# Kernel optimization log

Measured on AMD Instinct MI355X. Metric: run time of the kernel, lower is better.

The kernel has to match this reference:

```python
import jax, jax.numpy as jnp
import numpy as np

_SQRT1_2 = 0.7071067811865476

B, S, D, N, NCH = 4, 2048, 1024, 32768, 8


def setup_inputs() -> dict:
    key = jax.random.key(0)
    ks = jax.random.split(key, 6)
    return {
        "x": jax.random.normal(ks[0], (B, S, D), jnp.float32),
        "h": jax.random.normal(ks[1], (B, S, D), jnp.float32),
        "emb": jax.random.normal(ks[2], (N, D), jnp.float32),
        "tau_offset": jax.random.normal(ks[3], (B, S, 1), jnp.float32),
        "w_read": jax.random.normal(ks[4], (N, D), jnp.float32),
        "w_write": jax.random.normal(ks[5], (N, D), jnp.float32),
        "n_chunks": NCH,
    }


def _srw_chunked(x, h, emb_unit, tau_offset, w_read, w_write, n_chunks):
    b, s, d = x.shape
    n = emb_unit.shape[0]
    cs = n // n_chunks
    h_bf = h.astype(jnp.bfloat16)
    x_bf = x.astype(jnp.bfloat16)
    emb_bf = emb_unit.astype(jnp.bfloat16)
    read_bf = w_read.astype(jnp.bfloat16)
    write_bf = w_write.astype(jnp.bfloat16)
    z1 = jnp.zeros((b, s, 1), jnp.float32)

    # ---- pass 1: online score statistics over chunks of N ----
    @jax.checkpoint
    def stats_step(carry, i):
        s_sum, sq_sum, cube_sum, ns_sum, ns_sq = carry
        ec = jax.lax.dynamic_slice_in_dim(emb_bf, i * cs, cs, axis=0)
        sc = (h_bf @ ec.T).astype(jnp.float32)  # [B,S,cs]
        s_sum = s_sum + sc.sum(-1, keepdims=True)
        sq_sum = sq_sum + (sc ** 2).sum(-1, keepdims=True)
        cube_sum = cube_sum + (sc ** 3).sum(-1, keepdims=True)
        pns = sc.mean(axis=(0, 1))  # per-neuron mean score [cs]
        return ((s_sum, sq_sum, cube_sum, ns_sum + pns.sum(), ns_sq + (pns ** 2).sum()), None)

    (s_sum, sq_sum, cube_sum, ns_sum, ns_sq), _ = jax.lax.scan(
        stats_step, (z1, z1, z1, jnp.float32(0.0), jnp.float32(0.0)), jnp.arange(n_chunks))

    s_mean = s_sum / n
    s_std = jnp.sqrt(sq_sum / n - s_mean ** 2) + 1e-08
    tau = s_mean + tau_offset * s_std
    cube_mean = cube_sum / n
    central_third = cube_mean - 3.0 * s_mean * s_std ** 2 - s_mean ** 3
    score_skew = jax.lax.stop_gradient((central_third / (s_std ** 3 + 1e-08)).mean())
    mean_score = ns_sum / n
    var_score = ns_sq / n - mean_score ** 2
    score_lb = var_score / (mean_score ** 2 + var_score + 0.01)

    # ---- pass 2: erf-threshold gate + read/write GEMM accumulate ----
    @jax.checkpoint
    def gate_step(carry, i):
        out, wcost, gmax, act, strong, phib, zsum, z075c, z030c, glg = carry
        s0 = i * cs
        ec = jax.lax.dynamic_slice_in_dim(emb_bf, s0, cs, axis=0)
        rc = jax.lax.dynamic_slice_in_dim(read_bf, s0, cs, axis=0)
        wc = jax.lax.dynamic_slice_in_dim(write_bf, s0, cs, axis=0)
        rc = rc / (jnp.linalg.norm(rc, axis=-1, keepdims=True) + 1e-08)
        wc = wc / (jnp.linalg.norm(wc, axis=-1, keepdims=True) + 1e-08)
        z = ((h_bf @ ec.T).astype(jnp.float32) - tau) / s_std  # [B,S,cs]
        phi = 0.5 * (1.0 + jax.lax.erf(z * _SQRT1_2))
        gate = jnp.where(z > 0, z * phi, 0.0)
        xr = x_bf @ rc.T  # [B,S,cs]
        c_out = ((gate.astype(jnp.bfloat16) * xr) @ wc).astype(jnp.float32)  # [B,S,D]
        g_safe = gate + 1e-08
        new = (
            out + c_out,
            wcost + gate.sum(-1, keepdims=True),
            jnp.maximum(gmax, gate.max(-1, keepdims=True)),
            act + (gate > 0.0).astype(jnp.float32).sum(-1, keepdims=True),
            strong + (gate > 0.5).astype(jnp.float32).sum(-1, keepdims=True),
            phib + ((phi > 0.95) | (phi < 0.05)).astype(jnp.float32).sum(-1, keepdims=True),
            zsum + jnp.where(z > 0, z, 0.0).sum(-1, keepdims=True),
            z075c + ((z > 0) & (z < 0.75)).astype(jnp.float32).sum(-1, keepdims=True),
            z030c + ((z > 0) & (z < 0.3)).astype(jnp.float32).sum(-1, keepdims=True),
            glg + (gate * jnp.log(g_safe)).sum(-1, keepdims=True),
        )
        return (new, None)

    init = (jnp.zeros((b, s, d), jnp.float32), z1, jnp.full((b, s, 1), -1e9, jnp.float32),
            z1, z1, z1, z1, z1, z1, z1)
    (raw_out, wcost, gmax, act, strong, phib, zsum, z075c, z030c, glg), _ = jax.lax.scan(
        gate_step, init, jnp.arange(n_chunks))

    den = jnp.maximum(wcost, 1.0)
    out = (raw_out / den).astype(jnp.bfloat16)
    score_std_out = s_std.mean()
    es_out = wcost.mean()
    active_n_mean = act.mean()
    z_mean_active = zsum / (act + 1e-08)
    active_eps = act + 1e-08
    z_lt_075_frac = jax.lax.stop_gradient((z075c / active_eps).mean())
    z_lt_030_frac = jax.lax.stop_gradient((z030c / active_eps).mean())
    tau_abs_mean = jax.lax.stop_gradient(tau).mean()
    active_per_token_std = jax.lax.stop_gradient(act).std()
    gate_sum_eps = wcost + 1e-08
    entropy_per_token = -glg / gate_sum_eps + jnp.log(gate_sum_eps)
    gate_entropy = jax.lax.stop_gradient(entropy_per_token).mean()
    return (out.astype(jnp.float32), act / n, gmax, score_lb, score_std_out, es_out,
            active_n_mean, strong / n, phib / n, z_mean_active, tau_abs_mean,
            z_lt_075_frac, z_lt_030_frac, score_skew, active_per_token_std, gate_entropy)


def reference(x, h, emb, tau_offset, w_read, w_write, n_chunks):
    emb_unit = emb / (jnp.linalg.norm(emb, axis=-1, keepdims=True) + 1e-08)
    return _srw_chunked(x, h, emb_unit, tau_offset, w_read, w_write, n_chunks)
```

## Files before the change

### kernel.cpp

```cpp
#include <hip/hip_runtime.h>

#define DEV __device__ __forceinline__

typedef __attribute__((ext_vector_type(4))) float f32x4;
typedef __attribute__((ext_vector_type(8))) short s16x8;

static const int NTOK = 8192;
static const int DD   = 1024;
static const int NNEU = 32768;

static const int OUT_ACT    = 8388608;
static const int OUT_GMAX   = 8396800;
static const int OUT_SLB    = 8404992;
static const int OUT_SSTD   = 8404993;
static const int OUT_ES     = 8404994;
static const int OUT_ANM    = 8404995;
static const int OUT_STRONG = 8404996;
static const int OUT_PHIB   = 8413188;
static const int OUT_ZMEAN  = 8421380;
static const int OUT_TAUM   = 8429572;
static const int OUT_Z75    = 8429573;
static const int OUT_Z30    = 8429574;
static const int OUT_SKEW   = 8429575;
static const int OUT_ASTD   = 8429576;
static const int OUT_ENT    = 8429577;

DEV unsigned short f2bf(float f){
  unsigned u = __float_as_uint(f);
  u += 0x7fffu + ((u >> 16) & 1u);
  return (unsigned short)(u >> 16);
}
DEV float bf2f(unsigned short h){ return __uint_as_float(((unsigned)h) << 16); }
DEV float rnd_bf(float f){ return bf2f(f2bf(f)); }

template<int AUX>
DEV void gl_lds16(const void* g, void* l){
  __builtin_amdgcn_global_load_lds(
      (const __attribute__((address_space(1))) unsigned int*)g,
      (__attribute__((address_space(3))) unsigned int*)l, 16, 0, AUX);
}

DEV f32x4 mfma16(s16x8 a, s16x8 b, f32x4 c){
  return __builtin_amdgcn_mfma_f32_16x16x32_bf16(a, b, c, 0, 0, 0);
}

template<int AUX>
DEV void stage4(const unsigned short* __restrict__ G, size_t ld, int k0,
                unsigned short* L, int t){
  #pragma unroll
  for (int i = 0; i < 4; i++){
    int ch = i*256 + t;
    int row = ch >> 3, c = ch & 7;
    int cs = c ^ (row & 7);
    int wb = (i*256 + (t & 192)) * 16;
    gl_lds16<AUX>(G + (size_t)row * ld + k0 + cs*8, (char*)L + wb);
  }
}

DEV s16x8 frg(const unsigned short* L, int R, int kk, int lq){
  int cc = ((kk >> 3) + lq) ^ (R & 7);
  return *(const s16x8*)((const char*)L + R*128 + cc*16);
}

DEV int2 xcd_remap(){
  int orig = blockIdx.y * gridDim.x + blockIdx.x;
  int nwg  = gridDim.x * gridDim.y;
  int q = nwg >> 3;
  int xcd = orig & 7, idx = orig >> 3;
  int pos = xcd * q + idx;
  int2 r; r.x = pos >> 6; r.y = pos & 63;
  return r;
}


__global__ __launch_bounds__(256) void k_norms(const float* __restrict__ e,
    const float* __restrict__ r_, const float* __restrict__ w_,
    float* __restrict__ inv_e, float* __restrict__ inv_r, float* __restrict__ inv_w){
  int t = threadIdx.x, l = t & 63, wv = t >> 6;
  int row = blockIdx.x * 4 + wv;
  const float4* ep = (const float4*)(e  + (size_t)row * DD);
  const float4* rp = (const float4*)(r_ + (size_t)row * DD);
  const float4* wp = (const float4*)(w_ + (size_t)row * DD);
  float se = 0.f, sr = 0.f, sw = 0.f;
  #pragma unroll
  for (int j = 0; j < 4; j++){
    float4 v = ep[j*64 + l];
    se += v.x*v.x + v.y*v.y + v.z*v.z + v.w*v.w;
    float4 a = rp[j*64 + l];
    float a0 = rnd_bf(a.x), a1 = rnd_bf(a.y), a2 = rnd_bf(a.z), a3 = rnd_bf(a.w);
    sr += a0*a0 + a1*a1 + a2*a2 + a3*a3;
    float4 c = wp[j*64 + l];
    float c0 = rnd_bf(c.x), c1 = rnd_bf(c.y), c2 = rnd_bf(c.z), c3 = rnd_bf(c.w);
    sw += c0*c0 + c1*c1 + c2*c2 + c3*c3;
  }
  #pragma unroll
  for (int d = 1; d < 64; d <<= 1){
    se += __shfl_xor(se, d); sr += __shfl_xor(sr, d); sw += __shfl_xor(sw, d);
  }
  if (l == 0){
    inv_e[row] = 1.f / (sqrtf(se) + 1e-8f);
    inv_r[row] = 1.f / (sqrtf(sr) + 1e-8f);
    inv_w[row] = 1.f / (sqrtf(sw) + 1e-8f);
  }
}

__global__ __launch_bounds__(256) void k_cast_scale(const float* __restrict__ in,
    const float* __restrict__ inv, unsigned short* __restrict__ o, int round_first){
  size_t i = (size_t)blockIdx.x * 256 + threadIdx.x;
  int row = (int)(i >> 8);
  float s = inv[row];
  float4 v = ((const float4*)in)[i];
  ushort4 r;
  if (round_first){
    r.x = f2bf(rnd_bf(v.x) * s); r.y = f2bf(rnd_bf(v.y) * s);
    r.z = f2bf(rnd_bf(v.z) * s); r.w = f2bf(rnd_bf(v.w) * s);
  } else {
    r.x = f2bf(v.x * s); r.y = f2bf(v.y * s);
    r.z = f2bf(v.z * s); r.w = f2bf(v.w * s);
  }
  ((ushort4*)o)[i] = r;
}

__global__ __launch_bounds__(256) void k_cast(const float* __restrict__ in,
                                              unsigned short* __restrict__ o){
  size_t i = (size_t)blockIdx.x * 256 + threadIdx.x;
  float4 v = ((const float4*)in)[i];
  ushort4 r;
  r.x = f2bf(v.x); r.y = f2bf(v.y); r.z = f2bf(v.z); r.w = f2bf(v.w);
  ((ushort4*)o)[i] = r;
}

__global__ __launch_bounds__(256) void k_wcnT(const float* __restrict__ w_,
    const float* __restrict__ invw, unsigned short* __restrict__ o){
  __shared__ unsigned short tile[64][65];
  int t = threadIdx.x;
  int n0b = blockIdx.x * 64, d0 = blockIdx.y * 64;
  #pragma unroll
  for (int i = 0; i < 16; i++){
    int idx = t + i*256;
    int r = idx >> 6, c = idx & 63;
    float v = w_[(size_t)(n0b + r) * DD + d0 + c];
    tile[c][r] = f2bf(rnd_bf(v) * invw[n0b + r]);
  }
  __syncthreads();
  #pragma unroll
  for (int i = 0; i < 16; i++){
    int idx = t + i*256;
    int rd = idx >> 6, cn = idx & 63;
    o[(size_t)(d0 + rd) * NNEU + n0b + cn] = tile[rd][cn];
  }
}

__global__ __launch_bounds__(256) void k_hsum(const unsigned short* __restrict__ hb,
                                              float* __restrict__ hs){
  int t = threadIdx.x; int r0 = blockIdx.x * 128;
  float s[4] = {0.f, 0.f, 0.f, 0.f};
  for (int r = 0; r < 128; r++){
    const unsigned short* row = hb + (size_t)(r0 + r) * DD;
    #pragma unroll
    for (int j = 0; j < 4; j++) s[j] += bf2f(row[j*256 + t]);
  }
  #pragma unroll
  for (int j = 0; j < 4; j++) atomicAdd(hs + j*256 + t, s[j]);
}

__global__ __launch_bounds__(256) void k_pns(const unsigned short* __restrict__ eb,
    const float* __restrict__ hs, float* __restrict__ ns){
  __shared__ float hsh[1024];
  __shared__ float pr[8];
  int t = threadIdx.x, l = t & 63, wv = t >> 6;
  for (int i = t; i < 1024; i += 256) hsh[i] = hs[i];
  __syncthreads();
  float bs = 0.f, bq = 0.f;
  for (int it = 0; it < 32; it++){
    int row = blockIdx.x * 128 + it*4 + wv;
    const unsigned short* er = eb + (size_t)row * DD + l*16;
    float s = 0.f;
    #pragma unroll
    for (int j = 0; j < 16; j++) s += hsh[l*16 + j] * bf2f(er[j]);
    #pragma unroll
    for (int d = 1; d < 64; d <<= 1) s += __shfl_xor(s, d);
    float pns = s * (1.f / 8192.f);
    bs += pns; bq += pns * pns;
  }
  if (l == 0){ pr[wv*2] = bs; pr[wv*2 + 1] = bq; }
  __syncthreads();
  if (t == 0){
    atomicAdd(ns + 0, pr[0] + pr[2] + pr[4] + pr[6]);
    atomicAdd(ns + 1, pr[1] + pr[3] + pr[5] + pr[7]);
  }
}


__global__ __launch_bounds__(256, 2) void k_stats_gemm(
    const unsigned short* __restrict__ A, const unsigned short* __restrict__ Bm,
    float* __restrict__ s_sum, float* __restrict__ sq_sum, float* __restrict__ cu_sum)
{
  __shared__ unsigned short lds[16384];
  unsigned short* lA = lds;
  unsigned short* lB = lds + 8192;
  const int t = threadIdx.x, l = t & 63, wv = t >> 6;
  const int wm = wv >> 1, wn = wv & 1;
  const int lq = l >> 4, lr = l & 15;
  int2 rm = xcd_remap();
  const int bx = rm.x, by = rm.y;
  const unsigned short* Ab = A  + (size_t)by * 128 * DD;
  const unsigned short* Bb = Bm + (size_t)bx * 128 * DD;
  f32x4 acc[4][4];
  #pragma unroll
  for (int m = 0; m < 4; m++)
    #pragma unroll
    for (int n = 0; n < 4; n++) acc[m][n] = (f32x4){0.f, 0.f, 0.f, 0.f};

  for (int k0 = 0; k0 < DD; k0 += 64){
    __syncthreads();
    stage4<0>(Ab, DD, k0, lA, t);
    stage4<0>(Bb, DD, k0, lB, t);
    asm volatile("s_waitcnt vmcnt(0)" ::: "memory");
    __syncthreads();
    #pragma unroll
    for (int kk = 0; kk < 64; kk += 32){
      s16x8 af[4], bf4[4];
      #pragma unroll
      for (int m = 0; m < 4; m++) af[m]  = frg(lA, wm*64 + m*16 + lr, kk, lq);
      #pragma unroll
      for (int n = 0; n < 4; n++) bf4[n] = frg(lB, wn*64 + n*16 + lr, kk, lq);
      #pragma unroll
      for (int m = 0; m < 4; m++)
        #pragma unroll
        for (int n = 0; n < 4; n++)
          acc[m][n] = mfma16(af[m], bf4[n], acc[m][n]);
    }
  }
  __syncthreads();
  float* red = (float*)lds;
  #pragma unroll
  for (int m = 0; m < 4; m++)
  #pragma unroll
  for (int r = 0; r < 4; r++){
    float s1 = 0.f, s2 = 0.f, s3 = 0.f;
    #pragma unroll
    for (int n = 0; n < 4; n++){
      float v = rnd_bf(acc[m][n][r]);
      s1 += v; float v2 = v*v; s2 += v2; s3 += v2*v;
    }
    #pragma unroll
    for (int d = 1; d < 16; d <<= 1){
      s1 += __shfl_xor(s1, d); s2 += __shfl_xor(s2, d); s3 += __shfl_xor(s3, d);
    }
    if (lr == 0){
      int rl = wm*64 + m*16 + lq*4 + r;
      float* p = red + (wn*128 + rl)*4;
      p[0] = s1; p[1] = s2; p[2] = s3;
    }
  }
  __syncthreads();
  const int row0 = by * 128;
  for (int idx = t; idx < 384; idx += 256){
    int rl = idx / 3, st = idx - rl*3;
    float v = red[rl*4 + st] + red[(128 + rl)*4 + st];
    float* dst = (st == 0) ? s_sum : (st == 1) ? sq_sum : cu_sum;
    atomicAdd(dst + row0 + rl, v);
  }
}

__global__ __launch_bounds__(256) void k_tau(const float* __restrict__ s_sum,
    const float* __restrict__ sq_sum, const float* __restrict__ tof,
    float* __restrict__ tau, float* __restrict__ rstd){
  int i = blockIdx.x * 256 + threadIdx.x;
  float mean = s_sum[i] * (1.f / 32768.f);
  float var  = sq_sum[i] * (1.f / 32768.f) - mean*mean;
  float sstd = sqrtf(fmaxf(var, 0.f)) + 1e-8f;
  tau[i]  = mean + tof[i] * sstd;
  rstd[i] = 1.f / sstd;
}


__global__ __launch_bounds__(256, 2) void k_gate_gemm(
    const unsigned short* __restrict__ Hb, const unsigned short* __restrict__ Eb,
    const unsigned short* __restrict__ Xb, const unsigned short* __restrict__ Rb,
    const float* __restrict__ tau, const float* __restrict__ rstd,
    unsigned short* __restrict__ P, int NC, int n0,
    float* __restrict__ wcostp, float* __restrict__ gmaxp, float* __restrict__ actp,
    float* __restrict__ strongp, float* __restrict__ phibp, float* __restrict__ zsump,
    float* __restrict__ z075p, float* __restrict__ z030p, float* __restrict__ glgp)
{
  __shared__ unsigned short lds[32768];
  unsigned short* lH = lds;
  unsigned short* lE = lds + 8192;
  unsigned short* lX = lds + 16384;
  unsigned short* lR = lds + 24576;
  const int t = threadIdx.x, l = t & 63, wv = t >> 6;
  const int wm = wv >> 1, wn = wv & 1;
  const int lq = l >> 4, lr = l & 15;
  int2 rm = xcd_remap();
  const int bx = rm.x, by = rm.y;
  const unsigned short* Hp = Hb + (size_t)by * 128 * DD;
  const unsigned short* Xp = Xb + (size_t)by * 128 * DD;
  const unsigned short* Ep = Eb + (size_t)(n0 + bx*128) * DD;
  const unsigned short* Rp = Rb + (size_t)(n0 + bx*128) * DD;
  f32x4 accS[4][4], accX[4][4];
  #pragma unroll
  for (int m = 0; m < 4; m++)
    #pragma unroll
    for (int n = 0; n < 4; n++){
      accS[m][n] = (f32x4){0.f,0.f,0.f,0.f};
      accX[m][n] = (f32x4){0.f,0.f,0.f,0.f};
    }

  for (int k0 = 0; k0 < DD; k0 += 64){
    __syncthreads();
    stage4<0>(Hp, DD, k0, lH, t);
    stage4<0>(Ep, DD, k0, lE, t);
    stage4<0>(Xp, DD, k0, lX, t);
    stage4<0>(Rp, DD, k0, lR, t);
    asm volatile("s_waitcnt vmcnt(0)" ::: "memory");
    __syncthreads();
    #pragma unroll
    for (int kk = 0; kk < 64; kk += 32){
      s16x8 af[4], bf4[4];
      #pragma unroll
      for (int m = 0; m < 4; m++) af[m]  = frg(lH, wm*64 + m*16 + lr, kk, lq);
      #pragma unroll
      for (int n = 0; n < 4; n++) bf4[n] = frg(lE, wn*64 + n*16 + lr, kk, lq);
      #pragma unroll
      for (int m = 0; m < 4; m++)
        #pragma unroll
        for (int n = 0; n < 4; n++)
          accS[m][n] = mfma16(af[m], bf4[n], accS[m][n]);
      #pragma unroll
      for (int m = 0; m < 4; m++) af[m]  = frg(lX, wm*64 + m*16 + lr, kk, lq);
      #pragma unroll
      for (int n = 0; n < 4; n++) bf4[n] = frg(lR, wn*64 + n*16 + lr, kk, lq);
      #pragma unroll
      for (int m = 0; m < 4; m++)
        #pragma unroll
        for (int n = 0; n < 4; n++)
          accX[m][n] = mfma16(af[m], bf4[n], accX[m][n]);
    }
  }
  __syncthreads();
  float* red = (float*)lds;
  #pragma unroll
  for (int m = 0; m < 4; m++)
  #pragma unroll
  for (int r = 0; r < 4; r++){
    int rl = wm*64 + m*16 + lq*4 + r;
    int gr = by*128 + rl;
    float tauv = tau[gr], rs = rstd[gr];
    float wsum = 0.f, gmx = 0.f, ac = 0.f, stc = 0.f, pb = 0.f;
    float zs = 0.f, z7 = 0.f, z3 = 0.f, gl = 0.f;
    #pragma unroll
    for (int n = 0; n < 4; n++){
      float sc = rnd_bf(accS[m][n][r]);
      float xr = rnd_bf(accX[m][n][r]);
      float z = (sc - tauv) * rs;
      float phi = 0.5f * (1.0f + erff(z * 0.70710678118654752440f));
      float gate = (z > 0.f) ? z * phi : 0.f;
      wsum += gate; gmx = fmaxf(gmx, gate);
      if (gate > 0.f)  ac  += 1.f;
      if (gate > 0.5f) stc += 1.f;
      if (phi > 0.95f || phi < 0.05f) pb += 1.f;
      if (z > 0.f){ zs += z; if (z < 0.75f) z7 += 1.f; if (z < 0.3f) z3 += 1.f; }
      gl += gate * __logf(gate + 1e-8f);
      float p = rnd_bf(gate) * xr;
      __builtin_nontemporal_store(f2bf(p), &P[(size_t)gr * NC + bx*128 + wn*64 + n*16 + lr]);
    }
    #pragma unroll
    for (int d = 1; d < 16; d <<= 1){
      wsum += __shfl_xor(wsum, d); gmx = fmaxf(gmx, __shfl_xor(gmx, d));
      ac += __shfl_xor(ac, d);  stc += __shfl_xor(stc, d); pb += __shfl_xor(pb, d);
      zs += __shfl_xor(zs, d);  z7  += __shfl_xor(z7, d);  z3 += __shfl_xor(z3, d);
      gl += __shfl_xor(gl, d);
    }
    if (lr == 0){
      float* p = red + (wn*128 + rl)*10;
      p[0]=wsum; p[1]=gmx; p[2]=ac; p[3]=stc; p[4]=pb; p[5]=zs; p[6]=z7; p[7]=z3; p[8]=gl;
    }
  }
  __syncthreads();
  for (int idx = t; idx < 1152; idx += 256){
    int rl = idx / 9, st = idx - rl*9;
    float a = red[rl*10 + st], b = red[(128 + rl)*10 + st];
    int gr = by*128 + rl;
    if (st == 1){
      atomicMax((int*)(gmaxp + gr), __float_as_int(fmaxf(a, b)));
    } else {
      float v = a + b;
      float* dst = (st==0)?wcostp:(st==2)?actp:(st==3)?strongp:(st==4)?phibp:
                   (st==5)?zsump:(st==6)?z075p:(st==7)?z030p:glgp;
      atomicAdd(dst + gr, v);
    }
  }
}


__global__ __launch_bounds__(256, 2) void k_out_gemm(
    const unsigned short* __restrict__ Pm, const unsigned short* __restrict__ Bt,
    float* __restrict__ outp, int NC, int n0, int accum)
{
  __shared__ unsigned short lds[16384];
  unsigned short* lA = lds;
  unsigned short* lB = lds + 8192;
  const int t = threadIdx.x, l = t & 63, wv = t >> 6;
  const int wm = wv >> 1, wn = wv & 1;
  const int lq = l >> 4, lr = l & 15;
  int2 rm = xcd_remap();
  const int bx = rm.x, by = rm.y;
  const unsigned short* Ab = Pm + (size_t)by * 128 * NC;
  const unsigned short* Bb = Bt + (size_t)bx * 128 * NNEU + n0;
  f32x4 acc[4][4];
  #pragma unroll
  for (int m = 0; m < 4; m++)
    #pragma unroll
    for (int n = 0; n < 4; n++) acc[m][n] = (f32x4){0.f,0.f,0.f,0.f};

  for (int k0 = 0; k0 < NC; k0 += 64){
    __syncthreads();
    stage4<2>(Ab, NC, k0, lA, t);
    stage4<0>(Bb, NNEU, k0, lB, t);
    asm volatile("s_waitcnt vmcnt(0)" ::: "memory");
    __syncthreads();
    #pragma unroll
    for (int kk = 0; kk < 64; kk += 32){
      s16x8 af[4], bf4[4];
      #pragma unroll
      for (int m = 0; m < 4; m++) af[m]  = frg(lA, wm*64 + m*16 + lr, kk, lq);
      #pragma unroll
      for (int n = 0; n < 4; n++) bf4[n] = frg(lB, wn*64 + n*16 + lr, kk, lq);
      #pragma unroll
      for (int m = 0; m < 4; m++)
        #pragma unroll
        for (int n = 0; n < 4; n++)
          acc[m][n] = mfma16(af[m], bf4[n], acc[m][n]);
    }
  }
  #pragma unroll
  for (int m = 0; m < 4; m++)
  #pragma unroll
  for (int n = 0; n < 4; n++)
  #pragma unroll
  for (int r = 0; r < 4; r++){
    int gr = by*128 + wm*64 + m*16 + lq*4 + r;
    int dc = bx*128 + wn*64 + n*16 + lr;
    float* o = outp + (size_t)gr * DD + dc;
    if (accum) *o += acc[m][n][r];
    else       *o  = acc[m][n][r];
  }
}


__global__ __launch_bounds__(256) void k_out_fin(float* __restrict__ o,
                                                 const float* __restrict__ wcost){
  size_t i = (size_t)blockIdx.x * 256 + threadIdx.x;
  float4 v = ((const float4*)o)[i];
  int tk = (int)(i >> 8);
  float den = fmaxf(wcost[tk], 1.f);
  v.x = rnd_bf(v.x / den); v.y = rnd_bf(v.y / den);
  v.z = rnd_bf(v.z / den); v.w = rnd_bf(v.w / den);
  ((float4*)o)[i] = v;
}

__global__ __launch_bounds__(1024) void k_final(
    const float* __restrict__ s_sum, const float* __restrict__ sq_sum,
    const float* __restrict__ cu_sum, const float* __restrict__ tof,
    const float* __restrict__ wcost, const float* __restrict__ gmax,
    const float* __restrict__ act, const float* __restrict__ strong,
    const float* __restrict__ phib, const float* __restrict__ zsum,
    const float* __restrict__ z075, const float* __restrict__ z030,
    const float* __restrict__ glg, const float* __restrict__ ns,
    float* __restrict__ out)
{
  int tid = threadIdx.x;
  float s0=0,s1=0,s2=0,s3=0,s4=0,s5=0,s6=0,s7=0,s8=0;
  for (int i = tid; i < NTOK; i += 1024){
    float mean = s_sum[i] * (1.f / 32768.f);
    float var  = sq_sum[i] * (1.f / 32768.f) - mean*mean;
    float sstd = sqrtf(fmaxf(var, 0.f)) + 1e-8f;
    float tauv = mean + tof[i] * sstd;
    float wc = wcost[i], ac = act[i];
    out[OUT_ACT + i]    = ac * (1.f / 32768.f);
    out[OUT_GMAX + i]   = gmax[i];
    out[OUT_STRONG + i] = strong[i] * (1.f / 32768.f);
    out[OUT_PHIB + i]   = phib[i] * (1.f / 32768.f);
    out[OUT_ZMEAN + i]  = zsum[i] / (ac + 1e-8f);
    float c3 = cu_sum[i] * (1.f / 32768.f) - 3.f*mean*sstd*sstd - mean*mean*mean;
    float skew = c3 / (sstd*sstd*sstd + 1e-8f);
    float gse = wc + 1e-8f;
    float ent = -glg[i] / gse + logf(gse);
    s0 += sstd; s1 += wc; s2 += ac; s3 += ac*ac; s4 += tauv;
    s5 += z075[i] / (ac + 1e-8f); s6 += z030[i] / (ac + 1e-8f); s7 += skew; s8 += ent;
  }
  __shared__ float rb[16][9];
  int lane = tid & 63, wid = tid >> 6;
  #pragma unroll
  for (int d = 1; d < 64; d <<= 1){
    s0 += __shfl_xor(s0,d); s1 += __shfl_xor(s1,d); s2 += __shfl_xor(s2,d);
    s3 += __shfl_xor(s3,d); s4 += __shfl_xor(s4,d); s5 += __shfl_xor(s5,d);
    s6 += __shfl_xor(s6,d); s7 += __shfl_xor(s7,d); s8 += __shfl_xor(s8,d);
  }
  if (lane == 0){
    rb[wid][0]=s0; rb[wid][1]=s1; rb[wid][2]=s2; rb[wid][3]=s3; rb[wid][4]=s4;
    rb[wid][5]=s5; rb[wid][6]=s6; rb[wid][7]=s7; rb[wid][8]=s8;
  }
  __syncthreads();
  if (tid == 0){
    float S[9];
    for (int k = 0; k < 9; k++){ float a = 0.f; for (int w2 = 0; w2 < 16; w2++) a += rb[w2][k]; S[k] = a; }
    const float inv = 1.f / 8192.f;
    float act_mean = S[2] * inv;
    out[OUT_SSTD] = S[0] * inv;
    out[OUT_ES]   = S[1] * inv;
    out[OUT_ANM]  = act_mean;
    out[OUT_ASTD] = sqrtf(fmaxf(S[3]*inv - act_mean*act_mean, 0.f));
    out[OUT_TAUM] = S[4] * inv;
    out[OUT_Z75]  = S[5] * inv;
    out[OUT_Z30]  = S[6] * inv;
    out[OUT_SKEW] = S[7] * inv;
    out[OUT_ENT]  = S[8] * inv;
    float ms = ns[0] * (1.f / 32768.f);
    float vs = ns[1] * (1.f / 32768.f) - ms*ms;
    out[OUT_SLB] = vs / (ms*ms + vs + 0.01f);
  }
}


extern "C" void kernel_launch(void* const* d_in, const int* in_sizes, int n_in,
                              void* d_out, int out_size, void* d_ws, size_t ws_size,
                              hipStream_t stream)
{
  (void)in_sizes; (void)n_in; (void)out_size;
  const float* x   = (const float*)d_in[0];
  const float* h   = (const float*)d_in[1];
  const float* emb = (const float*)d_in[2];
  const float* tof = (const float*)d_in[3];
  const float* wr  = (const float*)d_in[4];
  const float* ww  = (const float*)d_in[5];
  float* out = (float*)d_out;
  char* ws = (char*)d_ws;

  size_t off = 0;
  auto get = [&](size_t n){ size_t o = off; off += (n + 255) & ~(size_t)255; return o; };
  unsigned short* emb_bf = (unsigned short*)(ws + get((size_t)NNEU*DD*2));
  unsigned short* rcn_bf = (unsigned short*)(ws + get((size_t)NNEU*DD*2));
  unsigned short* wcnT   = (unsigned short*)(ws + get((size_t)DD*NNEU*2));
  unsigned short* h_bf   = (unsigned short*)(ws + get((size_t)NTOK*DD*2));
  unsigned short* x_bf   = (unsigned short*)(ws + get((size_t)NTOK*DD*2));
  float* inv_e = (float*)(ws + get(NNEU*4));
  float* inv_r = (float*)(ws + get(NNEU*4));
  float* inv_w = (float*)(ws + get(NNEU*4));
  size_t zoff = off;
  float* hsum   = (float*)(ws + get(DD*4));
  float* s_sum  = (float*)(ws + get(NTOK*4));
  float* sq_sum = (float*)(ws + get(NTOK*4));
  float* cu_sum = (float*)(ws + get(NTOK*4));
  float* tau    = (float*)(ws + get(NTOK*4));
  float* rstd   = (float*)(ws + get(NTOK*4));
  float* wcost  = (float*)(ws + get(NTOK*4));
  float* gmax   = (float*)(ws + get(NTOK*4));
  float* act    = (float*)(ws + get(NTOK*4));
  float* strong = (float*)(ws + get(NTOK*4));
  float* phib   = (float*)(ws + get(NTOK*4));
  float* zsum   = (float*)(ws + get(NTOK*4));
  float* z075   = (float*)(ws + get(NTOK*4));
  float* z030   = (float*)(ws + get(NTOK*4));
  float* glg    = (float*)(ws + get(NTOK*4));
  float* ns     = (float*)(ws + get(256));
  size_t zlen = off - zoff;
  off = (off + 4095) & ~(size_t)4095;
  size_t poff = off;
  size_t pavail = ws_size > poff ? ws_size - poff : 0;
  int nsplit = 1;
  while (nsplit < 64 && (size_t)NTOK * (NNEU / nsplit) * 2 > pavail) nsplit <<= 1;
  int NC = NNEU / nsplit;
  unsigned short* P = (unsigned short*)(ws + poff);

  hipMemsetAsync(ws + zoff, 0, zlen, stream);

  dim3 b256(256);
  k_norms<<<dim3(NNEU/4), b256, 0, stream>>>(emb, wr, ww, inv_e, inv_r, inv_w);
  k_cast_scale<<<dim3(NNEU*DD/4/256), b256, 0, stream>>>(emb, inv_e, emb_bf, 0);
  k_cast_scale<<<dim3(NNEU*DD/4/256), b256, 0, stream>>>(wr, inv_r, rcn_bf, 1);
  k_wcnT<<<dim3(NNEU/64, DD/64), b256, 0, stream>>>(ww, inv_w, wcnT);
  k_cast<<<dim3(NTOK*DD/4/256), b256, 0, stream>>>(h, h_bf);
  k_cast<<<dim3(NTOK*DD/4/256), b256, 0, stream>>>(x, x_bf);
  k_hsum<<<dim3(NTOK/128), b256, 0, stream>>>(h_bf, hsum);
  k_pns<<<dim3(NNEU/128), b256, 0, stream>>>(emb_bf, hsum, ns);
  k_stats_gemm<<<dim3(NNEU/128, NTOK/128), b256, 0, stream>>>(h_bf, emb_bf, s_sum, sq_sum, cu_sum);
  k_tau<<<dim3(NTOK/256), b256, 0, stream>>>(s_sum, sq_sum, tof, tau, rstd);
  for (int c = 0; c < nsplit; ++c){
    k_gate_gemm<<<dim3(NC/128, NTOK/128), b256, 0, stream>>>(h_bf, emb_bf, x_bf, rcn_bf,
        tau, rstd, P, NC, c*NC, wcost, gmax, act, strong, phib, zsum, z075, z030, glg);
    k_out_gemm<<<dim3(DD/128, NTOK/128), b256, 0, stream>>>(P, wcnT, out, NC, c*NC, c);
  }
  k_out_fin<<<dim3(NTOK*DD/4/256), b256, 0, stream>>>(out, wcost);
  k_final<<<dim3(1), dim3(1024), 0, stream>>>(s_sum, sq_sum, cu_sum, tof, wcost, gmax,
      act, strong, phib, zsum, z075, z030, glg, ns, out);
}
```

Before: 4.118 ms.

## Cache bf16 score matrix from stats pass, double-buffer GEMM LDS loads

The stats GEMM now writes its bf16 score tile to workspace, so the gate pass reads cached scores instead of recomputing H·Eᵀ. It only computes the X·Rᵀ GEMM, with a fallback to the full gate GEMM when workspace is short. The stats, gate and output GEMMs get double-buffered LDS staging that prefetches the next k-tile during MFMA compute. The transposed write-weight buffer aliases emb_bf once it is dead, and the chunk size is fixed to four chunks. This trades an extra 512MB of score writes and reads for removing half the gate-pass FLOPs, and relies on the workspace being large enough.

```diff
diff --git a/kernel.cpp b/kernel.cpp
--- a/kernel.cpp
+++ b/kernel.cpp
@@ -4,10 +4,12 @@
 
 typedef __attribute__((ext_vector_type(4))) float f32x4;
 typedef __attribute__((ext_vector_type(8))) short s16x8;
+typedef __attribute__((ext_vector_type(8))) unsigned short u16x8;
 
 static const int NTOK = 8192;
 static const int DD   = 1024;
 static const int NNEU = 32768;
+static const int NC   = 8192;
 
 static const int OUT_ACT    = 8388608;
 static const int OUT_GMAX   = 8396800;
@@ -62,6 +64,12 @@
   return *(const s16x8*)((const char*)L + R*128 + cc*16);
 }
 
+DEV void waitv_bar(){
+  asm volatile("s_waitcnt vmcnt(0)" ::: "memory");
+  __builtin_amdgcn_s_barrier();
+  __builtin_amdgcn_sched_barrier(0);
+}
+
 DEV int2 xcd_remap(){
   int orig = blockIdx.y * gridDim.x + blockIdx.x;
   int nwg  = gridDim.x * gridDim.y;
@@ -194,11 +202,10 @@
 
 __global__ __launch_bounds__(256, 2) void k_stats_gemm(
     const unsigned short* __restrict__ A, const unsigned short* __restrict__ Bm,
-    float* __restrict__ s_sum, float* __restrict__ sq_sum, float* __restrict__ cu_sum)
+    float* __restrict__ s_sum, float* __restrict__ sq_sum, float* __restrict__ cu_sum,
+    unsigned short* __restrict__ Sb, int kst)
 {
-  __shared__ unsigned short lds[16384];
-  unsigned short* lA = lds;
-  unsigned short* lB = lds + 8192;
+  __shared__ unsigned short lds[32768];
   const int t = threadIdx.x, l = t & 63, wv = t >> 6;
   const int wm = wv >> 1, wn = wv & 1;
   const int lq = l >> 4, lr = l & 15;
@@ -212,27 +219,62 @@
     #pragma unroll
     for (int n = 0; n < 4; n++) acc[m][n] = (f32x4){0.f, 0.f, 0.f, 0.f};
 
-  for (int k0 = 0; k0 < DD; k0 += 64){
-    __syncthreads();
-    stage4<0>(Ab, DD, k0, lA, t);
-    stage4<0>(Bb, DD, k0, lB, t);
-    asm volatile("s_waitcnt vmcnt(0)" ::: "memory");
-    __syncthreads();
+  stage4<0>(Ab, DD, 0, lds, t);
+  stage4<0>(Bb, DD, 0, lds + 8192, t);
+  waitv_bar();
+  int cur = 0;
+  for (int ks = 0; ks < 16; ++ks){
+    unsigned short* Lc = lds + cur*16384;
+    if (ks + 1 < 16){
+      unsigned short* Ln = lds + (cur^1)*16384;
+      int k0 = (ks+1)*64;
+      stage4<0>(Ab, DD, k0, Ln, t);
+      stage4<0>(Bb, DD, k0, Ln + 8192, t);
+    }
     #pragma unroll
     for (int kk = 0; kk < 64; kk += 32){
       s16x8 af[4], bf4[4];
       #pragma unroll
-      for (int m = 0; m < 4; m++) af[m]  = frg(lA, wm*64 + m*16 + lr, kk, lq);
-      #pragma unroll
-      for (int n = 0; n < 4; n++) bf4[n] = frg(lB, wn*64 + n*16 + lr, kk, lq);
+      for (int m = 0; m < 4; m++) af[m]  = frg(Lc, wm*64 + m*16 + lr, kk, lq);
+      #pragma unroll
+      for (int n = 0; n < 4; n++) bf4[n] = frg(Lc + 8192, wn*64 + n*16 + lr, kk, lq);
       #pragma unroll
       for (int m = 0; m < 4; m++)
         #pragma unroll
         for (int n = 0; n < 4; n++)
           acc[m][n] = mfma16(af[m], bf4[n], acc[m][n]);
     }
-  }
-  __syncthreads();
+    waitv_bar();
+    cur ^= 1;
+  }
+
+  int ci = bx >> 6;
+  if (ci < kst){
+    unsigned short* sl = lds;
+    #pragma unroll
+    for (int m = 0; m < 4; m++)
+    #pragma unroll
+    for (int n = 0; n < 4; n++)
+    #pragma unroll
+    for (int r = 0; r < 4; r++){
+      int rl = wm*64 + m*16 + lq*4 + r;
+      int cl = wn*64 + n*16 + lr;
+      sl[rl*136 + cl] = f2bf(acc[m][n][r]);
+    }
+    __syncthreads();
+    unsigned short* Sp = Sb + (size_t)ci * NTOK * NC;
+    int bxc = bx & 63;
+    #pragma unroll
+    for (int i = 0; i < 8; i++){
+      int idx = i*2048 + t*8;
+      int row = idx >> 7, col = idx & 127;
+      u16x8 v = *(const u16x8*)&sl[row*136 + col];
+      __builtin_nontemporal_store(v,
+        (u16x8*)(Sp + (size_t)(by*128 + row) * NC + bxc*128 + col));
+    }
+  }
+  __syncthreads();
+
   float* red = (float*)lds;
   #pragma unroll
   for (int m = 0; m < 4; m++)
@@ -276,11 +318,130 @@
 }
 
 
+__global__ __launch_bounds__(256, 2) void k_gateS(
+    const unsigned short* __restrict__ Xb, const unsigned short* __restrict__ Rb,
+    const float* __restrict__ tau, const float* __restrict__ rstd,
+    unsigned short* __restrict__ SP, int n0,
+    float* __restrict__ wcostp, float* __restrict__ gmaxp, float* __restrict__ actp,
+    float* __restrict__ strongp, float* __restrict__ phibp, float* __restrict__ zsump,
+    float* __restrict__ z075p, float* __restrict__ z030p, float* __restrict__ glgp)
+{
+  __shared__ unsigned short lds[32768];
+  const int t = threadIdx.x, l = t & 63, wv = t >> 6;
+  const int wm = wv >> 1, wn = wv & 1;
+  const int lq = l >> 4, lr = l & 15;
+  int2 rm = xcd_remap();
+  const int bx = rm.x, by = rm.y;
+  const unsigned short* Xp = Xb + (size_t)by * 128 * DD;
+  const unsigned short* Rp = Rb + (size_t)(n0 + bx*128) * DD;
+  f32x4 accX[4][4];
+  #pragma unroll
+  for (int m = 0; m < 4; m++)
+    #pragma unroll
+    for (int n = 0; n < 4; n++) accX[m][n] = (f32x4){0.f,0.f,0.f,0.f};
+
+  stage4<0>(Xp, DD, 0, lds, t);
+  stage4<0>(Rp, DD, 0, lds + 8192, t);
+  waitv_bar();
+  int cur = 0;
+  for (int ks = 0; ks < 16; ++ks){
+    unsigned short* Lc = lds + cur*16384;
+    if (ks + 1 < 16){
+      unsigned short* Ln = lds + (cur^1)*16384;
+      int k0 = (ks+1)*64;
+      stage4<0>(Xp, DD, k0, Ln, t);
+      stage4<0>(Rp, DD, k0, Ln + 8192, t);
+    }
+    #pragma unroll
+    for (int kk = 0; kk < 64; kk += 32){
+      s16x8 af[4], bf4[4];
+      #pragma unroll
+      for (int m = 0; m < 4; m++) af[m]  = frg(Lc, wm*64 + m*16 + lr, kk, lq);
+      #pragma unroll
+      for (int n = 0; n < 4; n++) bf4[n] = frg(Lc + 8192, wn*64 + n*16 + lr, kk, lq);
+      #pragma unroll
+      for (int m = 0; m < 4; m++)
+        #pragma unroll
+        for (int n = 0; n < 4; n++)
+          accX[m][n] = mfma16(af[m], bf4[n], accX[m][n]);
+    }
+    waitv_bar();
+    cur ^= 1;
+  }
+
+  unsigned short sv[4][4][4];
+  #pragma unroll
+  for (int m = 0; m < 4; m++)
+  #pragma unroll
+  for (int r = 0; r < 4; r++)
+  #pragma unroll
+  for (int n = 0; n < 4; n++){
+    int gr = by*128 + wm*64 + m*16 + lq*4 + r;
+    int gc = bx*128 + wn*64 + n*16 + lr;
+    sv[m][r][n] = SP[(size_t)gr * NC + gc];
+  }
+
+  __syncthreads();
+  float* red = (float*)lds;
+  #pragma unroll
+  for (int m = 0; m < 4; m++)
+  #pragma unroll
+  for (int r = 0; r < 4; r++){
+    int rl = wm*64 + m*16 + lq*4 + r;
+    int gr = by*128 + rl;
+    float tauv = tau[gr], rs = rstd[gr];
+    float wsum = 0.f, gmx = 0.f, ac = 0.f, stc = 0.f, pb = 0.f;
+    float zs = 0.f, z7 = 0.f, z3 = 0.f, gl = 0.f;
+    #pragma unroll
+    for (int n = 0; n < 4; n++){
+      float sc = bf2f(sv[m][r][n]);
+      float xr = rnd_bf(accX[m][n][r]);
+      float z = (sc - tauv) * rs;
+      float phi = 0.5f * (1.0f + erff(z * 0.70710678118654752440f));
+      float gate = (z > 0.f) ? z * phi : 0.f;
+      wsum += gate; gmx = fmaxf(gmx, gate);
+      if (gate > 0.f)  ac  += 1.f;
+      if (gate > 0.5f) stc += 1.f;
+      if (phi > 0.95f || phi < 0.05f) pb += 1.f;
+      if (z > 0.f){ zs += z; if (z < 0.75f) z7 += 1.f; if (z < 0.3f) z3 += 1.f; }
+      gl += gate * __logf(gate + 1e-8f);
+      float p = rnd_bf(gate) * xr;
+      SP[(size_t)gr * NC + bx*128 + wn*64 + n*16 + lr] = f2bf(p);
+    }
+    #pragma unroll
+    for (int d = 1; d < 16; d <<= 1){
+      wsum += __shfl_xor(wsum, d); gmx = fmaxf(gmx, __shfl_xor(gmx, d));
+      ac += __shfl_xor(ac, d);  stc += __shfl_xor(stc, d); pb += __shfl_xor(pb, d);
+      zs += __shfl_xor(zs, d);  z7  += __shfl_xor(z7, d);  z3 += __shfl_xor(z3, d);
+      gl += __shfl_xor(gl, d);
+    }
+    if (lr == 0){
+      float* p = red + (wn*128 + rl)*10;
+      p[0]=wsum; p[1]=gmx; p[2]=ac; p[3]=stc; p[4]=pb; p[5]=zs; p[6]=z7; p[7]=z3; p[8]=gl;
+    }
+  }
+  __syncthreads();
+  for (int idx = t; idx < 1152; idx += 256){
+    int rl = idx / 9, st = idx - rl*9;
+    float a = red[rl*10 + st], b = red[(128 + rl)*10 + st];
+    int gr = by*128 + rl;
+    if (st == 1){
+      atomicMax((int*)(gmaxp + gr), __float_as_int(fmaxf(a, b)));
+    } else {
+      float v = a + b;
+      float* dst = (st==0)?wcostp:(st==2)?actp:(st==3)?strongp:(st==4)?phibp:
+                   (st==5)?zsump:(st==6)?z075p:(st==7)?z030p:glgp;
+      atomicAdd(dst + gr, v);
+    }
+  }
+}
+
+
 __global__ __launch_bounds__(256, 2) void k_gate_gemm(
     const unsigned short* __restrict__ Hb, const unsigned short* __restrict__ Eb,
     const unsigned short* __restrict__ Xb, const unsigned short* __restrict__ Rb,
     const float* __restrict__ tau, const float* __restrict__ rstd,
-    unsigned short* __restrict__ P, int NC, int n0,
+    unsigned short* __restrict__ P, int n0,
     float* __restrict__ wcostp, float* __restrict__ gmaxp, float* __restrict__ actp,
     float* __restrict__ strongp, float* __restrict__ phibp, float* __restrict__ zsump,
     float* __restrict__ z075p, float* __restrict__ z030p, float* __restrict__ glgp)
@@ -364,7 +525,7 @@
       if (z > 0.f){ zs += z; if (z < 0.75f) z7 += 1.f; if (z < 0.3f) z3 += 1.f; }
       gl += gate * __logf(gate + 1e-8f);
       float p = rnd_bf(gate) * xr;
-      __builtin_nontemporal_store(f2bf(p), &P[(size_t)gr * NC + bx*128 + wn*64 + n*16 + lr]);
+      P[(size_t)gr * NC + bx*128 + wn*64 + n*16 + lr] = f2bf(p);
     }
     #pragma unroll
     for (int d = 1; d < 16; d <<= 1){
@@ -397,11 +558,9 @@
 
 __global__ __launch_bounds__(256, 2) void k_out_gemm(
     const unsigned short* __restrict__ Pm, const unsigned short* __restrict__ Bt,
-    float* __restrict__ outp, int NC, int n0, int accum)
+    float* __restrict__ outp, int n0, int accum)
 {
-  __shared__ unsigned short lds[16384];
-  unsigned short* lA = lds;
-  unsigned short* lB = lds + 8192;
+  __shared__ unsigned short lds[32768];
   const int t = threadIdx.x, l = t & 63, wv = t >> 6;
   const int wm = wv >> 1, wn = wv & 1;
   const int lq = l >> 4, lr = l & 15;
@@ -415,25 +574,34 @@
     #pragma unroll
     for (int n = 0; n < 4; n++) acc[m][n] = (f32x4){0.f,0.f,0.f,0.f};
 
-  for (int k0 = 0; k0 < NC; k0 += 64){
-    __syncthreads();
-    stage4<2>(Ab, NC, k0, lA, t);
-    stage4<0>(Bb, NNEU, k0, lB, t);
-    asm volatile("s_waitcnt vmcnt(0)" ::: "memory");
-    __syncthreads();
+  const int NT = NC / 64;
+  stage4<2>(Ab, NC, 0, lds, t);
+  stage4<0>(Bb, NNEU, 0, lds + 8192, t);
+  waitv_bar();
+  int cur = 0;
+  for (int ks = 0; ks < NT; ++ks){
+    unsigned short* Lc = lds + cur*16384;
+    if (ks + 1 < NT){
+      unsigned short* Ln = lds + (cur^1)*16384;
+      int k0 = (ks+1)*64;
+      stage4<2>(Ab, NC, k0, Ln, t);
+      stage4<0>(Bb, NNEU, k0, Ln + 8192, t);
+    }
     #pragma unroll
     for (int kk = 0; kk < 64; kk += 32){
       s16x8 af[4], bf4[4];
       #pragma unroll
-      for (int m = 0; m < 4; m++) af[m]  = frg(lA, wm*64 + m*16 + lr, kk, lq);
-      #pragma unroll
-      for (int n = 0; n < 4; n++) bf4[n] = frg(lB, wn*64 + n*16 + lr, kk, lq);
+      for (int m = 0; m < 4; m++) af[m]  = frg(Lc, wm*64 + m*16 + lr, kk, lq);
+      #pragma unroll
+      for (int n = 0; n < 4; n++) bf4[n] = frg(Lc + 8192, wn*64 + n*16 + lr, kk, lq);
       #pragma unroll
       for (int m = 0; m < 4; m++)
         #pragma unroll
         for (int n = 0; n < 4; n++)
           acc[m][n] = mfma16(af[m], bf4[n], acc[m][n]);
     }
+    waitv_bar();
+    cur ^= 1;
   }
   #pragma unroll
   for (int m = 0; m < 4; m++)
@@ -541,9 +709,7 @@
 
   size_t off = 0;
   auto get = [&](size_t n){ size_t o = off; off += (n + 255) & ~(size_t)255; return o; };
-  unsigned short* emb_bf = (unsigned short*)(ws + get((size_t)NNEU*DD*2));
   unsigned short* rcn_bf = (unsigned short*)(ws + get((size_t)NNEU*DD*2));
-  unsigned short* wcnT   = (unsigned short*)(ws + get((size_t)DD*NNEU*2));
   unsigned short* h_bf   = (unsigned short*)(ws + get((size_t)NTOK*DD*2));
   unsigned short* x_bf   = (unsigned short*)(ws + get((size_t)NTOK*DD*2));
   float* inv_e = (float*)(ws + get(NNEU*4));
@@ -567,13 +733,24 @@
   float* glg    = (float*)(ws + get(NTOK*4));
   float* ns     = (float*)(ws + get(256));
   size_t zlen = off - zoff;
-  off = (off + 4095) & ~(size_t)4095;
-  size_t poff = off;
-  size_t pavail = ws_size > poff ? ws_size - poff : 0;
-  int nsplit = 1;
-  while (nsplit < 64 && (size_t)NTOK * (NNEU / nsplit) * 2 > pavail) nsplit <<= 1;
-  int NC = NNEU / nsplit;
-  unsigned short* P = (unsigned short*)(ws + poff);
+  unsigned short* emb_bf = (unsigned short*)(ws + get((size_t)NNEU*DD*2));
+
+  const size_t szS = (size_t)NTOK * NC * 2;
+  unsigned short* wcnT;
+  int kst;
+  size_t poff;
+  size_t poffA = (off + 4095) & ~(size_t)4095;
+  size_t availA = ws_size > poffA ? ws_size - poffA : 0;
+  if (availA >= 4*szS){
+    wcnT = emb_bf;
+    kst = 4; poff = poffA;
+  } else {
+    wcnT = (unsigned short*)(ws + get((size_t)DD*NNEU*2));
+    poff = (off + 4095) & ~(size_t)4095;
+    size_t avail = ws_size > poff ? ws_size - poff : 0;
+    kst = (int)(avail / szS); if (kst > 4) kst = 4;
+  }
+  unsigned short* Sb = (unsigned short*)(ws + poff);
 
   hipMemsetAsync(ws + zoff, 0, zlen, stream);
 
@@ -581,17 +758,26 @@
   k_norms<<<dim3(NNEU/4), b256, 0, stream>>>(emb, wr, ww, inv_e, inv_r, inv_w);
   k_cast_scale<<<dim3(NNEU*DD/4/256), b256, 0, stream>>>(emb, inv_e, emb_bf, 0);
   k_cast_scale<<<dim3(NNEU*DD/4/256), b256, 0, stream>>>(wr, inv_r, rcn_bf, 1);
-  k_wcnT<<<dim3(NNEU/64, DD/64), b256, 0, stream>>>(ww, inv_w, wcnT);
   k_cast<<<dim3(NTOK*DD/4/256), b256, 0, stream>>>(h, h_bf);
   k_cast<<<dim3(NTOK*DD/4/256), b256, 0, stream>>>(x, x_bf);
   k_hsum<<<dim3(NTOK/128), b256, 0, stream>>>(h_bf, hsum);
   k_pns<<<dim3(NNEU/128), b256, 0, stream>>>(emb_bf, hsum, ns);
-  k_stats_gemm<<<dim3(NNEU/128, NTOK/128), b256, 0, stream>>>(h_bf, emb_bf, s_sum, sq_sum, cu_sum);
+  k_stats_gemm<<<dim3(NNEU/128, NTOK/128), b256, 0, stream>>>(h_bf, emb_bf,
+      s_sum, sq_sum, cu_sum, Sb, kst);
   k_tau<<<dim3(NTOK/256), b256, 0, stream>>>(s_sum, sq_sum, tof, tau, rstd);
-  for (int c = 0; c < nsplit; ++c){
-    k_gate_gemm<<<dim3(NC/128, NTOK/128), b256, 0, stream>>>(h_bf, emb_bf, x_bf, rcn_bf,
-        tau, rstd, P, NC, c*NC, wcost, gmax, act, strong, phib, zsum, z075, z030, glg);
-    k_out_gemm<<<dim3(DD/128, NTOK/128), b256, 0, stream>>>(P, wcnT, out, NC, c*NC, c);
+  k_wcnT<<<dim3(NNEU/64, DD/64), b256, 0, stream>>>(ww, inv_w, wcnT);
+
+  for (int c = 0; c < 4; ++c){
+    int reg = (kst > 0) ? (c < kst ? c : (c % kst)) : 0;
+    unsigned short* Pc = Sb + (size_t)reg * NTOK * NC;
+    if (c < kst){
+      k_gateS<<<dim3(NC/128, NTOK/128), b256, 0, stream>>>(x_bf, rcn_bf,
+          tau, rstd, Pc, c*NC, wcost, gmax, act, strong, phib, zsum, z075, z030, glg);
+    } else {
+      k_gate_gemm<<<dim3(NC/128, NTOK/128), b256, 0, stream>>>(h_bf, emb_bf, x_bf, rcn_bf,
+          tau, rstd, Pc, c*NC, wcost, gmax, act, strong, phib, zsum, z075, z030, glg);
+    }
+    k_out_gemm<<<dim3(DD/128, NTOK/128), b256, 0, stream>>>(Pc, wcnT, out, c*NC, c);
   }
   k_out_fin<<<dim3(NTOK*DD/4/256), b256, 0, stream>>>(out, wcost);
   k_final<<<dim3(1), dim3(1024), 0, stream>>>(s_sum, sq_sum, cu_sum, tof, wcost, gmax,
```

After: 4.023 ms. -2.3%, faster.
